# Performance work log

Measured on AMD Instinct MI355X. Metric: run time of the kernel, lower is better.

## Reference

```python
import jax, jax.numpy as jnp
import numpy as np

N_NODES = 100000


def gcn_conv(x, edge_index, W, b):
    # PyG GCNConv: add self-loops, symmetric normalization D^-1/2 (A+I) D^-1/2
    src, dst = edge_index[0], edge_index[1]
    n = x.shape[0]
    ones = jnp.ones(src.shape[0], dtype=x.dtype)
    deg = jax.ops.segment_sum(ones, dst, num_segments=n) + 1.0  # +1 self-loop
    dinv = jax.lax.rsqrt(deg)
    h = x @ W  # transform first (smaller gather traffic when out_dim < in_dim)
    norm = dinv[src] * dinv[dst]  # [E]
    msg = h[src] * norm[:, None]  # [E, out]
    agg = jax.ops.segment_sum(msg, dst, num_segments=n)
    agg = agg + h * (dinv * dinv)[:, None]  # self-loop contribution
    return agg + b


def setup_inputs() -> dict:
    key = jax.random.key(0)
    k = jax.random.split(key, 8)
    feature_size = 128
    n_edges = 3200000
    x = jax.random.normal(k[0], (N_NODES, feature_size), dtype=jnp.float32)
    edge_index = jax.random.randint(k[1], (2, n_edges), 0, N_NODES, dtype=jnp.int64)
    # Glorot-ish params
    W1 = jax.random.normal(k[2], (feature_size, 64), dtype=jnp.float32) / np.sqrt(feature_size)
    b1 = jnp.zeros((64,), dtype=jnp.float32)
    W2 = jax.random.normal(k[3], (64, 128), dtype=jnp.float32) / np.sqrt(64)
    b2 = jnp.zeros((128,), dtype=jnp.float32)
    Wfc = jax.random.normal(k[4], (128, 1), dtype=jnp.float32) / np.sqrt(128)
    bfc = jnp.zeros((1,), dtype=jnp.float32)
    return {"x": x, "edge_index": edge_index, "W1": W1, "b1": b1,
            "W2": W2, "b2": b2, "Wfc": Wfc, "bfc": bfc}


def reference(x, edge_index, W1, b1, W2, b2, Wfc, bfc):
    h = jax.nn.relu(gcn_conv(x, edge_index, W1, b1))
    h = jax.nn.relu(gcn_conv(h, edge_index, W2, b2))
    return h @ Wfc + bfc  # [N, 1]
```

## Files before the change

kernel.cpp:

```cpp
#include <hip/hip_runtime.h>
#include <hip/hip_fp16.h>

#define NN 100000
#define NBIN 256
#define RANGE 391
#define CAP 16384
#define CAPL 16384

typedef _Float16 f16x8 __attribute__((ext_vector_type(8)));
typedef float f32x4 __attribute__((ext_vector_type(4)));

__device__ __forceinline__ void gemm1_tile(char* smem, int tile,
                                           const float* __restrict__ X,
                                           const float* __restrict__ W,
                                           __half* __restrict__ H, int n, int t) {
    constexpr int K = 128, C = 64, RPT = 2, CG = 16, RT = 64, XS = K + 4;
    float* Ws = (float*)smem;
    float* Xs = (float*)(smem + 32768);

    for (int i = t * 4; i < K * C; i += 2048)
        *(float4*)&Ws[i] = *(const float4*)&W[i];

    const int row0 = tile * RT;
    for (int i = t * 4; i < RT * K; i += 2048) {
        int r = i / K, k = i % K;
        int gr = row0 + r;
        float4 v = make_float4(0.f, 0.f, 0.f, 0.f);
        if (gr < n) v = *(const float4*)&X[(long long)gr * K + k];
        *(float4*)&Xs[r * XS + k] = v;
    }
    __syncthreads();

    const int cg = t % CG, rs = t / CG;
    float acc[RPT][4];
#pragma unroll
    for (int i = 0; i < RPT; ++i)
#pragma unroll
        for (int j = 0; j < 4; ++j) acc[i][j] = 0.f;

#pragma unroll 2
    for (int k4 = 0; k4 < K / 4; ++k4) {
        float4 xv[RPT];
#pragma unroll
        for (int i = 0; i < RPT; ++i)
            xv[i] = *(float4*)&Xs[(rs * RPT + i) * XS + k4 * 4];
#pragma unroll
        for (int j = 0; j < 4; ++j) {
            float4 w = *(float4*)&Ws[(k4 * 4 + j) * C + cg * 4];
#pragma unroll
            for (int i = 0; i < RPT; ++i) {
                float xvj = (&xv[i].x)[j];
                acc[i][0] = fmaf(xvj, w.x, acc[i][0]);
                acc[i][1] = fmaf(xvj, w.y, acc[i][1]);
                acc[i][2] = fmaf(xvj, w.z, acc[i][2]);
                acc[i][3] = fmaf(xvj, w.w, acc[i][3]);
            }
        }
    }
#pragma unroll
    for (int i = 0; i < RPT; ++i) {
        int gr = row0 + rs * RPT + i;
        if (gr < n) {
            union { __half h[4]; uint2 u; } pk;
            pk.h[0] = __float2half(acc[i][0]);
            pk.h[1] = __float2half(acc[i][1]);
            pk.h[2] = __float2half(acc[i][2]);
            pk.h[3] = __float2half(acc[i][3]);
            *(uint2*)&H[(long long)gr * C + cg * 4] = pk.u;
        }
    }
}

__global__ __launch_bounds__(512) void k_binA_gemm1(
        const int* __restrict__ ei_lo, int E,
        int* __restrict__ g_bincnt, unsigned* __restrict__ binbuf,
        const float* __restrict__ X, const float* __restrict__ W1,
        __half* __restrict__ H, int n, int nBA) {
    __shared__ alignas(16) char smem[66560];
    const int t = threadIdx.x;
    const int b = blockIdx.x;
    const bool isBin = ((b & 1) == 0) && ((b >> 1) < nBA);
    if (isBin) {
        const int blk = b >> 1;
        int* cnt   = (int*)smem;
        int* basep = (int*)(smem + 1024);
        int* pos   = (int*)(smem + 2048);
        int* pis64 = (int*)(smem + 3072);
        if (t < NBIN) { cnt[t] = 0; pos[t] = 0; }
        if (t == 0) {
            const unsigned* u = (const unsigned*)ei_lo;
            int is64 = 1;
            for (int i = 0; i < 64; ++i)
                if (u[2 * i + 1] != 0u) { is64 = 0; break; }
            *pis64 = is64;
        }
        __syncthreads();
        const int s = (*pis64) ? 2 : 1;
        constexpr int ITER = 16;
        const int base = blk * (512 * ITER);
        unsigned pk[ITER];
        int bn[ITER];
#pragma unroll
        for (int i = 0; i < ITER; ++i) {
            int e = base + i * 512 + t;
            if (e < E) {
                int src = __builtin_nontemporal_load(&ei_lo[(long long)s * e]);
                int dst = __builtin_nontemporal_load(&ei_lo[(long long)s * (E + e)]);
                int bb = dst / RANGE;
                bn[i] = bb;
                pk[i] = ((unsigned)(dst - bb * RANGE) << 17) | (unsigned)src;
                atomicAdd(&cnt[bb], 1);
            } else bn[i] = -1;
        }
        __syncthreads();
        if (t < NBIN) basep[t] = atomicAdd(&g_bincnt[t], cnt[t]);
        __syncthreads();
#pragma unroll
        for (int i = 0; i < ITER; ++i) {
            if (bn[i] >= 0) {
                int r = atomicAdd(&pos[bn[i]], 1);
                binbuf[(long long)bn[i] * CAP + basep[bn[i]] + r] = pk[i];
            }
        }
    } else {
        gemm1_tile(smem, b >> 1, X, W1, H, n, t);
    }
}

__global__ __launch_bounds__(512) void k_build_gemm1(
        const unsigned* __restrict__ binbuf, const int* __restrict__ g_bincnt,
        int* __restrict__ row_ptr, float* __restrict__ dinv, int* __restrict__ csr,
        int n, int E,
        const float* __restrict__ X, const float* __restrict__ W1,
        __half* __restrict__ H, int tile0) {
    __shared__ alignas(16) char smem[69632];
    const int t = threadIdx.x;
    if ((int)blockIdx.x < NBIN) {
        unsigned* ebuf = (unsigned*)smem;
        int* cnt  = (int*)(smem + 65536);
        int* ssum = (int*)(smem + 67584);
        int* pref = (int*)(smem + 68608);
        const int bin = blockIdx.x;
        const int lo = bin * RANGE;
        const int rn = min(RANGE, n - lo);
        const int nE = min(g_bincnt[bin], CAPL);
        const unsigned* __restrict__ src = binbuf + (long long)bin * CAP;

        cnt[t] = 0;
        if (t < NBIN) pref[t] = g_bincnt[t];
        __syncthreads();

        for (int i = t; i < nE; i += 512) {
            unsigned e = src[i];
            ebuf[i] = e;
            atomicAdd(&cnt[(int)(e >> 17)], 1);
        }
        __syncthreads();

        for (int off = 1; off < NBIN; off <<= 1) {
            int add = (t >= off && t < NBIN) ? pref[t - off] : 0;
            __syncthreads();
            if (t < NBIN) pref[t] += add;
            __syncthreads();
        }
        const int bstart = (bin > 0) ? pref[bin - 1] : 0;

        int a = 0, bcnt = 0;
        if (t < 256) { a = cnt[2 * t]; bcnt = cnt[2 * t + 1]; ssum[t] = a + bcnt; }
        __syncthreads();
        for (int off = 1; off < 256; off <<= 1) {
            int add = (t >= off && t < 256) ? ssum[t - off] : 0;
            __syncthreads();
            if (t < 256) ssum[t] += add;
            __syncthreads();
        }
        if (t < 256) {
            int prev = (t > 0) ? ssum[t - 1] : 0;
            cnt[2 * t] = prev;
            cnt[2 * t + 1] = prev + a;
            if (2 * t < rn) {
                row_ptr[lo + 2 * t] = bstart + prev;
                dinv[lo + 2 * t] = rsqrtf((float)a + 1.f);
            }
            if (2 * t + 1 < rn) {
                row_ptr[lo + 2 * t + 1] = bstart + prev + a;
                dinv[lo + 2 * t + 1] = rsqrtf((float)bcnt + 1.f);
            }
        }
        if (bin == NBIN - 1 && t == 0) row_ptr[n] = E;
        __syncthreads();

        for (int i = t; i < nE; i += 512) {
            unsigned e = ebuf[i];
            int slot = bstart + atomicAdd(&cnt[(int)(e >> 17)], 1);
            csr[slot] = (int)(e & 0x1FFFFu);
        }
    } else {
        gemm1_tile(smem, tile0 + ((int)blockIdx.x - NBIN), X, W1, H, n, t);
    }
}

__global__ __launch_bounds__(256) void k_scale(__half* __restrict__ h,
                                               const float* __restrict__ dinv, int n8) {
    int idx = blockIdx.x * 256 + threadIdx.x;
    if (idx >= n8) return;
    float d = dinv[idx >> 3];
    uint4 u = *(uint4*)&h[(long long)idx * 8];
    union { __half hh[8]; uint4 u; } o;
    float2 f;
    f = __half22float2(*(__half2*)&u.x); o.hh[0] = __float2half(f.x * d); o.hh[1] = __float2half(f.y * d);
    f = __half22float2(*(__half2*)&u.y); o.hh[2] = __float2half(f.x * d); o.hh[3] = __float2half(f.y * d);
    f = __half22float2(*(__half2*)&u.z); o.hh[4] = __float2half(f.x * d); o.hh[5] = __float2half(f.y * d);
    f = __half22float2(*(__half2*)&u.w); o.hh[6] = __float2half(f.x * d); o.hh[7] = __float2half(f.y * d);
    *(uint4*)&h[(long long)idx * 8] = o.u;
}

template <bool RELU>
__global__ __launch_bounds__(256) void k_gather(const __half* __restrict__ h,
                                                const int* __restrict__ row_ptr,
                                                const int* __restrict__ csr,
                                                const float* __restrict__ dinv,
                                                const float* __restrict__ bias,
                                                __half* __restrict__ out, int n) {
    const int node = blockIdx.x * 4 + (threadIdx.x >> 6);
    if (node >= n) return;
    const int lane = threadIdx.x & 63;
    const int g = lane >> 3;
    const int fl = lane & 7;
    const float d = dinv[node];
    const int beg = row_ptr[node], end = row_ptr[node + 1];
    const int last = end - 1;
    const int zrow = n;

    uint4 su = make_uint4(0u, 0u, 0u, 0u);
    if (g == 0) su = *(const uint4*)&h[(long long)node * 64 + fl * 8];

    __half2 z = __float2half2_rn(0.f);
    __half2 acc0 = z, acc1 = z, acc2 = z, acc3 = z;

    for (int base = beg; base < end; base += 32) {
        int e0 = base + g, e1 = base + 8 + g, e2 = base + 16 + g, e3 = base + 24 + g;
        int c0 = csr[min(e0, last)];
        int c1 = csr[min(e1, last)];
        int c2 = csr[min(e2, last)];
        int c3 = csr[min(e3, last)];
        int s0 = (e0 < end) ? c0 : zrow;
        int s1 = (e1 < end) ? c1 : zrow;
        int s2 = (e2 < end) ? c2 : zrow;
        int s3 = (e3 < end) ? c3 : zrow;
        uint4 u0 = *(const uint4*)&h[(long long)s0 * 64 + fl * 8];
        uint4 u1 = *(const uint4*)&h[(long long)s1 * 64 + fl * 8];
        uint4 u2 = *(const uint4*)&h[(long long)s2 * 64 + fl * 8];
        uint4 u3 = *(const uint4*)&h[(long long)s3 * 64 + fl * 8];
        __half2 p0 = __hadd2(*(__half2*)&u0.x, *(__half2*)&u1.x);
        __half2 q0 = __hadd2(*(__half2*)&u2.x, *(__half2*)&u3.x);
        acc0 = __hadd2(acc0, __hadd2(p0, q0));
        __half2 p1 = __hadd2(*(__half2*)&u0.y, *(__half2*)&u1.y);
        __half2 q1 = __hadd2(*(__half2*)&u2.y, *(__half2*)&u3.y);
        acc1 = __hadd2(acc1, __hadd2(p1, q1));
        __half2 p2 = __hadd2(*(__half2*)&u0.z, *(__half2*)&u1.z);
        __half2 q2 = __hadd2(*(__half2*)&u2.z, *(__half2*)&u3.z);
        acc2 = __hadd2(acc2, __hadd2(p2, q2));
        __half2 p3 = __hadd2(*(__half2*)&u0.w, *(__half2*)&u1.w);
        __half2 q3 = __hadd2(*(__half2*)&u2.w, *(__half2*)&u3.w);
        acc3 = __hadd2(acc3, __hadd2(p3, q3));
    }

    float2 f0 = __half22float2(acc0);
    float2 f1 = __half22float2(acc1);
    float2 f2 = __half22float2(acc2);
    float2 f3 = __half22float2(acc3);
    float r0 = f0.x, r1 = f0.y, r2 = f1.x, r3 = f1.y;
    float r4 = f2.x, r5 = f2.y, r6 = f3.x, r7 = f3.y;
#pragma unroll
    for (int off = 8; off <= 32; off <<= 1) {
        r0 += __shfl_xor(r0, off, 64);
        r1 += __shfl_xor(r1, off, 64);
        r2 += __shfl_xor(r2, off, 64);
        r3 += __shfl_xor(r3, off, 64);
        r4 += __shfl_xor(r4, off, 64);
        r5 += __shfl_xor(r5, off, 64);
        r6 += __shfl_xor(r6, off, 64);
        r7 += __shfl_xor(r7, off, 64);
    }
    if (g == 0) {
        float2 s0 = __half22float2(*(__half2*)&su.x);
        float2 s1 = __half22float2(*(__half2*)&su.y);
        float2 s2 = __half22float2(*(__half2*)&su.z);
        float2 s3 = __half22float2(*(__half2*)&su.w);
        r0 += s0.x; r1 += s0.y; r2 += s1.x; r3 += s1.y;
        r4 += s2.x; r5 += s2.y; r6 += s3.x; r7 += s3.y;
        union { __half hh[8]; uint4 u; } o;
        if (RELU) {
            float4 bv0 = *(const float4*)&bias[fl * 8];
            float4 bv1 = *(const float4*)&bias[fl * 8 + 4];
            o.hh[0] = __float2half(fmaxf(fmaf(d, r0, bv0.x), 0.f) * d);
            o.hh[1] = __float2half(fmaxf(fmaf(d, r1, bv0.y), 0.f) * d);
            o.hh[2] = __float2half(fmaxf(fmaf(d, r2, bv0.z), 0.f) * d);
            o.hh[3] = __float2half(fmaxf(fmaf(d, r3, bv0.w), 0.f) * d);
            o.hh[4] = __float2half(fmaxf(fmaf(d, r4, bv1.x), 0.f) * d);
            o.hh[5] = __float2half(fmaxf(fmaf(d, r5, bv1.y), 0.f) * d);
            o.hh[6] = __float2half(fmaxf(fmaf(d, r6, bv1.z), 0.f) * d);
            o.hh[7] = __float2half(fmaxf(fmaf(d, r7, bv1.w), 0.f) * d);
        } else {
            o.hh[0] = __float2half(d * r0);
            o.hh[1] = __float2half(d * r1);
            o.hh[2] = __float2half(d * r2);
            o.hh[3] = __float2half(d * r3);
            o.hh[4] = __float2half(d * r4);
            o.hh[5] = __float2half(d * r5);
            o.hh[6] = __float2half(d * r6);
            o.hh[7] = __float2half(d * r7);
        }
        *(uint4*)&out[(long long)node * 64 + fl * 8] = o.u;
    }
}

__global__ __launch_bounds__(256) void k_gemm2fc(const __half* __restrict__ G,
                                                 const float* __restrict__ W2,
                                                 const float* __restrict__ b2,
                                                 const float* __restrict__ Wfc,
                                                 const float* __restrict__ bfc,
                                                 float* __restrict__ out, int n) {
    __shared__ __align__(16) _Float16 W2T[128][72];
    __shared__ float b2s[128], wfs[128];
    const int t = threadIdx.x;
    for (int i = t; i < 64 * 128; i += 256) {
        int k = i >> 7, c = i & 127;
        W2T[c][k] = (_Float16)W2[i];
    }
    if (t < 128) { b2s[t] = b2[t]; wfs[t] = Wfc[t]; }
    __syncthreads();

    const int w = t >> 6;
    const int l = t & 63;
    const int c16 = l & 15;
    const int q = l >> 4;
    const int row0 = blockIdx.x * 64 + w * 16;
    const int ar = row0 + c16;

    const _Float16* Gf = (const _Float16*)G;
    f16x8 a0 = {}, a1 = {};
    if (ar < n) {
        a0 = *(const f16x8*)&Gf[(long long)ar * 64 + q * 8];
        a1 = *(const f16x8*)&Gf[(long long)ar * 64 + 32 + q * 8];
    }

    float p0 = 0.f, p1 = 0.f, p2 = 0.f, p3 = 0.f;
#pragma unroll
    for (int ct = 0; ct < 8; ++ct) {
        f16x8 b0 = *(const f16x8*)&W2T[ct * 16 + c16][q * 8];
        f16x8 b1 = *(const f16x8*)&W2T[ct * 16 + c16][32 + q * 8];
        f32x4 acc = {0.f, 0.f, 0.f, 0.f};
        acc = __builtin_amdgcn_mfma_f32_16x16x32_f16(a0, b0, acc, 0, 0, 0);
        acc = __builtin_amdgcn_mfma_f32_16x16x32_f16(a1, b1, acc, 0, 0, 0);
        int col = ct * 16 + c16;
        float bb = b2s[col], wf = wfs[col];
        p0 += fmaxf(acc[0] + bb, 0.f) * wf;
        p1 += fmaxf(acc[1] + bb, 0.f) * wf;
        p2 += fmaxf(acc[2] + bb, 0.f) * wf;
        p3 += fmaxf(acc[3] + bb, 0.f) * wf;
    }
#pragma unroll
    for (int off = 1; off <= 8; off <<= 1) {
        p0 += __shfl_xor(p0, off, 64);
        p1 += __shfl_xor(p1, off, 64);
        p2 += __shfl_xor(p2, off, 64);
        p3 += __shfl_xor(p3, off, 64);
    }
    if (c16 == 0) {
        int row = row0 + q * 4;
        float bf = bfc[0];
        if (row < n)     out[row]     = p0 + bf;
        if (row + 1 < n) out[row + 1] = p1 + bf;
        if (row + 2 < n) out[row + 2] = p2 + bf;
        if (row + 3 < n) out[row + 3] = p3 + bf;
    }
}

extern "C" void kernel_launch(void* const* d_in, const int* in_sizes, int n_in,
                              void* d_out, int out_size, void* d_ws, size_t ws_size,
                              hipStream_t stream) {
    const float* x   = (const float*)d_in[0];
    const void*  ei  = d_in[1];
    const float* W1  = (const float*)d_in[2];
    const float* b1  = (const float*)d_in[3];
    const float* W2  = (const float*)d_in[4];
    const float* b2  = (const float*)d_in[5];
    const float* Wfc = (const float*)d_in[6];
    const float* bfc = (const float*)d_in[7];
    float* out = (float*)d_out;

    const int N = NN;
    const int E = in_sizes[1] / 2;

    char* ws = (char*)d_ws;
    size_t o = 0;
    auto carve = [&](size_t bytes) {
        char* p = ws + o;
        o = (o + bytes + 255) & ~(size_t)255;
        return p;
    };
    float*    dinv      = (float*)carve((size_t)N * 4);
    int*      row_ptr   = (int*)carve((size_t)(N + 1) * 4);
    int*      g_bincnt  = (int*)carve((size_t)NBIN * 4);
    int*      csr       = (int*)carve((size_t)E * 4);
    unsigned* binbuf    = (unsigned*)carve((size_t)NBIN * CAP * 4);
    __half*   bufA      = (__half*)carve((size_t)(N + 1) * 64 * 2);
    __half*   bufB      = (__half*)carve((size_t)(N + 1) * 64 * 2);
    __half*   bufG      = (__half*)carve((size_t)N * 64 * 2);

    const int* ei_lo = (const int*)ei;

    const int BA    = (E + 8191) / 8192;
    const int TILES = (N + 63) / 64;
    const int T1    = (BA - 1 < TILES) ? (BA - 1) : TILES;

    hipMemsetAsync(g_bincnt, 0, (size_t)NBIN * 4, stream);
    hipMemsetAsync(bufA + (size_t)N * 64, 0, 128, stream);
    hipMemsetAsync(bufB + (size_t)N * 64, 0, 128, stream);
    k_binA_gemm1<<<BA + T1, 512, 0, stream>>>(ei_lo, E, g_bincnt, binbuf,
                                              x, W1, bufA, N, BA);
    k_build_gemm1<<<NBIN + (TILES - T1), 512, 0, stream>>>(binbuf, g_bincnt,
                                                           row_ptr, dinv, csr, N, E,
                                                           x, W1, bufA, T1);
    k_scale<<<(N * 8 + 255) / 256, 256, 0, stream>>>(bufA, dinv, N * 8);

    k_gather<true><<<(N + 3) / 4, 256, 0, stream>>>(bufA, row_ptr, csr, dinv, b1, bufB, N);
    k_gather<false><<<(N + 3) / 4, 256, 0, stream>>>(bufB, row_ptr, csr, dinv, nullptr, bufG, N);
    k_gemm2fc<<<(N + 63) / 64, 256, 0, stream>>>(bufG, W2, b2, Wfc, bfc, out, N);
}
```

Measured before the change: 219.5 us.

## Unfuse GEMM1 from binning kernels and fold dinv scaling into GEMM1 epilogue

Splits the previously co-scheduled binning/CSR-build and GEMM1 blocks into separate kernels, then runs GEMM1 after the degree computation so it can multiply each output row by dinv before writing fp16. This removes the separate k_scale pass (one full read and write of H) and the heterogeneous-block kernels, which needed large shared allocations. The cost is that GEMM1 no longer overlaps with the binning and CSR build, and binning blocks shrink to 256 threads.

```diff
diff --git a/kernel.cpp b/kernel.cpp
--- a/kernel.cpp
+++ b/kernel.cpp
@@ -10,19 +10,134 @@
 typedef _Float16 f16x8 __attribute__((ext_vector_type(8)));
 typedef float f32x4 __attribute__((ext_vector_type(4)));
 
-__device__ __forceinline__ void gemm1_tile(char* smem, int tile,
-                                           const float* __restrict__ X,
-                                           const float* __restrict__ W,
-                                           __half* __restrict__ H, int n, int t) {
-    constexpr int K = 128, C = 64, RPT = 2, CG = 16, RT = 64, XS = K + 4;
-    float* Ws = (float*)smem;
-    float* Xs = (float*)(smem + 32768);
-
-    for (int i = t * 4; i < K * C; i += 2048)
+__global__ __launch_bounds__(256) void k_binA(const int* __restrict__ ei_lo,
+                                              int E, int* __restrict__ g_bincnt,
+                                              unsigned* __restrict__ binbuf) {
+    constexpr int ITER = 16;
+    __shared__ int cnt[NBIN], basep[NBIN], pos[NBIN];
+    __shared__ int s_is64;
+    const int t = threadIdx.x;
+    const int base = blockIdx.x * (256 * ITER);
+
+    cnt[t] = 0; pos[t] = 0;
+    if (t == 0) {
+        const unsigned* u = (const unsigned*)ei_lo;
+        int is64 = 1;
+        for (int i = 0; i < 64; ++i)
+            if (u[2 * i + 1] != 0u) { is64 = 0; break; }
+        s_is64 = is64;
+    }
+    __syncthreads();
+    const int s = s_is64 ? 2 : 1;
+
+    unsigned pk[ITER];
+    int bn[ITER];
+#pragma unroll
+    for (int i = 0; i < ITER; ++i) {
+        int e = base + i * 256 + t;
+        if (e < E) {
+            int src = __builtin_nontemporal_load(&ei_lo[(long long)s * e]);
+            int dst = __builtin_nontemporal_load(&ei_lo[(long long)s * (E + e)]);
+            int b = dst / RANGE;
+            bn[i] = b;
+            pk[i] = ((unsigned)(dst - b * RANGE) << 17) | (unsigned)src;
+            atomicAdd(&cnt[b], 1);
+        } else bn[i] = -1;
+    }
+    __syncthreads();
+    basep[t] = atomicAdd(&g_bincnt[t], cnt[t]);
+    __syncthreads();
+#pragma unroll
+    for (int i = 0; i < ITER; ++i) {
+        if (bn[i] >= 0) {
+            int r = atomicAdd(&pos[bn[i]], 1);
+            binbuf[(long long)bn[i] * CAP + basep[bn[i]] + r] = pk[i];
+        }
+    }
+}
+
+__global__ __launch_bounds__(512) void k_build(const unsigned* __restrict__ binbuf,
+                                               const int* __restrict__ g_bincnt,
+                                               int* __restrict__ row_ptr,
+                                               float* __restrict__ dinv,
+                                               int* __restrict__ csr, int n, int E) {
+    __shared__ unsigned ebuf[CAPL];
+    __shared__ int cnt[512];
+    __shared__ int ssum[256];
+    __shared__ int pref[NBIN];
+    const int t = threadIdx.x;
+    const int bin = blockIdx.x;
+    const int lo = bin * RANGE;
+    const int rn = min(RANGE, n - lo);
+    const int nE = min(g_bincnt[bin], CAPL);
+    const unsigned* __restrict__ src = binbuf + (long long)bin * CAP;
+
+    cnt[t] = 0;
+    if (t < NBIN) pref[t] = g_bincnt[t];
+    __syncthreads();
+
+    for (int i = t; i < nE; i += 512) {
+        unsigned e = src[i];
+        ebuf[i] = e;
+        atomicAdd(&cnt[(int)(e >> 17)], 1);
+    }
+    __syncthreads();
+
+    for (int off = 1; off < NBIN; off <<= 1) {
+        int add = (t >= off && t < NBIN) ? pref[t - off] : 0;
+        __syncthreads();
+        if (t < NBIN) pref[t] += add;
+        __syncthreads();
+    }
+    const int bstart = (bin > 0) ? pref[bin - 1] : 0;
+
+    int a = 0, bcnt = 0;
+    if (t < 256) { a = cnt[2 * t]; bcnt = cnt[2 * t + 1]; ssum[t] = a + bcnt; }
+    __syncthreads();
+    for (int off = 1; off < 256; off <<= 1) {
+        int add = (t >= off && t < 256) ? ssum[t - off] : 0;
+        __syncthreads();
+        if (t < 256) ssum[t] += add;
+        __syncthreads();
+    }
+    if (t < 256) {
+        int prev = (t > 0) ? ssum[t - 1] : 0;
+        cnt[2 * t] = prev;
+        cnt[2 * t + 1] = prev + a;
+        if (2 * t < rn) {
+            row_ptr[lo + 2 * t] = bstart + prev;
+            dinv[lo + 2 * t] = rsqrtf((float)a + 1.f);
+        }
+        if (2 * t + 1 < rn) {
+            row_ptr[lo + 2 * t + 1] = bstart + prev + a;
+            dinv[lo + 2 * t + 1] = rsqrtf((float)bcnt + 1.f);
+        }
+    }
+    if (bin == NBIN - 1 && t == 0) row_ptr[n] = E;
+    __syncthreads();
+
+    for (int i = t; i < nE; i += 512) {
+        unsigned e = ebuf[i];
+        int slot = bstart + atomicAdd(&cnt[(int)(e >> 17)], 1);
+        csr[slot] = (int)(e & 0x1FFFFu);
+    }
+}
+
+__global__ __launch_bounds__(256) void k_gemm1(const float* __restrict__ X,
+                                               const float* __restrict__ W,
+                                               const float* __restrict__ dinv,
+                                               __half* __restrict__ H, int n) {
+    constexpr int K = 128, C = 64, RPT = 2;
+    constexpr int CG = C / 4, RS = 256 / CG, RT = RS * RPT, XS = K + 4;
+    __shared__ float Ws[K * C];
+    __shared__ float Xs[RT * XS];
+    const int t = threadIdx.x;
+
+    for (int i = t * 4; i < K * C; i += 1024)
         *(float4*)&Ws[i] = *(const float4*)&W[i];
 
-    const int row0 = tile * RT;
-    for (int i = t * 4; i < RT * K; i += 2048) {
+    const int row0 = blockIdx.x * RT;
+    for (int i = t * 4; i < RT * K; i += 1024) {
         int r = i / K, k = i % K;
         int gr = row0 + r;
         float4 v = make_float4(0.f, 0.f, 0.f, 0.f);
@@ -61,158 +176,15 @@
     for (int i = 0; i < RPT; ++i) {
         int gr = row0 + rs * RPT + i;
         if (gr < n) {
+            float sc = dinv[gr];
             union { __half h[4]; uint2 u; } pk;
-            pk.h[0] = __float2half(acc[i][0]);
-            pk.h[1] = __float2half(acc[i][1]);
-            pk.h[2] = __float2half(acc[i][2]);
-            pk.h[3] = __float2half(acc[i][3]);
+            pk.h[0] = __float2half(acc[i][0] * sc);
+            pk.h[1] = __float2half(acc[i][1] * sc);
+            pk.h[2] = __float2half(acc[i][2] * sc);
+            pk.h[3] = __float2half(acc[i][3] * sc);
             *(uint2*)&H[(long long)gr * C + cg * 4] = pk.u;
         }
     }
-}
-
-__global__ __launch_bounds__(512) void k_binA_gemm1(
-        const int* __restrict__ ei_lo, int E,
-        int* __restrict__ g_bincnt, unsigned* __restrict__ binbuf,
-        const float* __restrict__ X, const float* __restrict__ W1,
-        __half* __restrict__ H, int n, int nBA) {
-    __shared__ alignas(16) char smem[66560];
-    const int t = threadIdx.x;
-    const int b = blockIdx.x;
-    const bool isBin = ((b & 1) == 0) && ((b >> 1) < nBA);
-    if (isBin) {
-        const int blk = b >> 1;
-        int* cnt   = (int*)smem;
-        int* basep = (int*)(smem + 1024);
-        int* pos   = (int*)(smem + 2048);
-        int* pis64 = (int*)(smem + 3072);
-        if (t < NBIN) { cnt[t] = 0; pos[t] = 0; }
-        if (t == 0) {
-            const unsigned* u = (const unsigned*)ei_lo;
-            int is64 = 1;
-            for (int i = 0; i < 64; ++i)
-                if (u[2 * i + 1] != 0u) { is64 = 0; break; }
-            *pis64 = is64;
-        }
-        __syncthreads();
-        const int s = (*pis64) ? 2 : 1;
-        constexpr int ITER = 16;
-        const int base = blk * (512 * ITER);
-        unsigned pk[ITER];
-        int bn[ITER];
-#pragma unroll
-        for (int i = 0; i < ITER; ++i) {
-            int e = base + i * 512 + t;
-            if (e < E) {
-                int src = __builtin_nontemporal_load(&ei_lo[(long long)s * e]);
-                int dst = __builtin_nontemporal_load(&ei_lo[(long long)s * (E + e)]);
-                int bb = dst / RANGE;
-                bn[i] = bb;
-                pk[i] = ((unsigned)(dst - bb * RANGE) << 17) | (unsigned)src;
-                atomicAdd(&cnt[bb], 1);
-            } else bn[i] = -1;
-        }
-        __syncthreads();
-        if (t < NBIN) basep[t] = atomicAdd(&g_bincnt[t], cnt[t]);
-        __syncthreads();
-#pragma unroll
-        for (int i = 0; i < ITER; ++i) {
-            if (bn[i] >= 0) {
-                int r = atomicAdd(&pos[bn[i]], 1);
-                binbuf[(long long)bn[i] * CAP + basep[bn[i]] + r] = pk[i];
-            }
-        }
-    } else {
-        gemm1_tile(smem, b >> 1, X, W1, H, n, t);
-    }
-}
-
-__global__ __launch_bounds__(512) void k_build_gemm1(
-        const unsigned* __restrict__ binbuf, const int* __restrict__ g_bincnt,
-        int* __restrict__ row_ptr, float* __restrict__ dinv, int* __restrict__ csr,
-        int n, int E,
-        const float* __restrict__ X, const float* __restrict__ W1,
-        __half* __restrict__ H, int tile0) {
-    __shared__ alignas(16) char smem[69632];
-    const int t = threadIdx.x;
-    if ((int)blockIdx.x < NBIN) {
-        unsigned* ebuf = (unsigned*)smem;
-        int* cnt  = (int*)(smem + 65536);
-        int* ssum = (int*)(smem + 67584);
-        int* pref = (int*)(smem + 68608);
-        const int bin = blockIdx.x;
-        const int lo = bin * RANGE;
-        const int rn = min(RANGE, n - lo);
-        const int nE = min(g_bincnt[bin], CAPL);
-        const unsigned* __restrict__ src = binbuf + (long long)bin * CAP;
-
-        cnt[t] = 0;
-        if (t < NBIN) pref[t] = g_bincnt[t];
-        __syncthreads();
-
-        for (int i = t; i < nE; i += 512) {
-            unsigned e = src[i];
-            ebuf[i] = e;
-            atomicAdd(&cnt[(int)(e >> 17)], 1);
-        }
-        __syncthreads();
-
-        for (int off = 1; off < NBIN; off <<= 1) {
-            int add = (t >= off && t < NBIN) ? pref[t - off] : 0;
-            __syncthreads();
-            if (t < NBIN) pref[t] += add;
-            __syncthreads();
-        }
-        const int bstart = (bin > 0) ? pref[bin - 1] : 0;
-
-        int a = 0, bcnt = 0;
-        if (t < 256) { a = cnt[2 * t]; bcnt = cnt[2 * t + 1]; ssum[t] = a + bcnt; }
-        __syncthreads();
-        for (int off = 1; off < 256; off <<= 1) {
-            int add = (t >= off && t < 256) ? ssum[t - off] : 0;
-            __syncthreads();
-            if (t < 256) ssum[t] += add;
-            __syncthreads();
-        }
-        if (t < 256) {
-            int prev = (t > 0) ? ssum[t - 1] : 0;
-            cnt[2 * t] = prev;
-            cnt[2 * t + 1] = prev + a;
-            if (2 * t < rn) {
-                row_ptr[lo + 2 * t] = bstart + prev;
-                dinv[lo + 2 * t] = rsqrtf((float)a + 1.f);
-            }
-            if (2 * t + 1 < rn) {
-                row_ptr[lo + 2 * t + 1] = bstart + prev + a;
-                dinv[lo + 2 * t + 1] = rsqrtf((float)bcnt + 1.f);
-            }
-        }
-        if (bin == NBIN - 1 && t == 0) row_ptr[n] = E;
-        __syncthreads();
-
-        for (int i = t; i < nE; i += 512) {
-            unsigned e = ebuf[i];
-            int slot = bstart + atomicAdd(&cnt[(int)(e >> 17)], 1);
-            csr[slot] = (int)(e & 0x1FFFFu);
-        }
-    } else {
-        gemm1_tile(smem, tile0 + ((int)blockIdx.x - NBIN), X, W1, H, n, t);
-    }
-}
-
-__global__ __launch_bounds__(256) void k_scale(__half* __restrict__ h,
-                                               const float* __restrict__ dinv, int n8) {
-    int idx = blockIdx.x * 256 + threadIdx.x;
-    if (idx >= n8) return;
-    float d = dinv[idx >> 3];
-    uint4 u = *(uint4*)&h[(long long)idx * 8];
-    union { __half hh[8]; uint4 u; } o;
-    float2 f;
-    f = __half22float2(*(__half2*)&u.x); o.hh[0] = __float2half(f.x * d); o.hh[1] = __float2half(f.y * d);
-    f = __half22float2(*(__half2*)&u.y); o.hh[2] = __float2half(f.x * d); o.hh[3] = __float2half(f.y * d);
-    f = __half22float2(*(__half2*)&u.z); o.hh[4] = __float2half(f.x * d); o.hh[5] = __float2half(f.y * d);
-    f = __half22float2(*(__half2*)&u.w); o.hh[6] = __float2half(f.x * d); o.hh[7] = __float2half(f.y * d);
-    *(uint4*)&h[(long long)idx * 8] = o.u;
 }
 
 template <bool RELU>
@@ -412,21 +384,16 @@
 
     const int* ei_lo = (const int*)ei;
 
-    const int BA    = (E + 8191) / 8192;
-    const int TILES = (N + 63) / 64;
-    const int T1    = (BA - 1 < TILES) ? (BA - 1) : TILES;
-
     hipMemsetAsync(g_bincnt, 0, (size_t)NBIN * 4, stream);
     hipMemsetAsync(bufA + (size_t)N * 64, 0, 128, stream);
     hipMemsetAsync(bufB + (size_t)N * 64, 0, 128, stream);
-    k_binA_gemm1<<<BA + T1, 512, 0, stream>>>(ei_lo, E, g_bincnt, binbuf,
-                                              x, W1, bufA, N, BA);
-    k_build_gemm1<<<NBIN + (TILES - T1), 512, 0, stream>>>(binbuf, g_bincnt,
-                                                           row_ptr, dinv, csr, N, E,
-                                                           x, W1, bufA, T1);
-    k_scale<<<(N * 8 + 255) / 256, 256, 0, stream>>>(bufA, dinv, N * 8);
-
+
+    k_binA<<<(E + 4095) / 4096, 256, 0, stream>>>(ei_lo, E, g_bincnt, binbuf);
+    k_build<<<NBIN, 512, 0, stream>>>(binbuf, g_bincnt, row_ptr, dinv, csr, N, E);
+
+    k_gemm1<<<(N + 31) / 32, 256, 0, stream>>>(x, W1, dinv, bufA, N);
     k_gather<true><<<(N + 3) / 4, 256, 0, stream>>>(bufA, row_ptr, csr, dinv, b1, bufB, N);
+
     k_gather<false><<<(N + 3) / 4, 256, 0, stream>>>(bufB, row_ptr, csr, dinv, nullptr, bufG, N);
     k_gemm2fc<<<(N + 63) / 64, 256, 0, stream>>>(bufG, W2, b2, Wfc, bfc, out, N);
 }
```

Result: no change. 217.7 us (-0.8%).
